# Optimization experiments

Hardware: AMD Instinct MI355X
Metric: run time of the kernel (lower is better)

The kernel has to match this reference:

```python
import jax, jax.numpy as jnp
from jax import lax
import numpy as np

B, T, F = 2048, 1000, 40
H1, H2 = 8, 6


def _p(key, shape, fan):
    # uniform(-1/sqrt(fan), 1/sqrt(fan)) like torch LSTM/Linear init
    bound = 1.0 / np.sqrt(fan)
    return jax.random.uniform(key, shape, jnp.float32, -bound, bound)


def setup_inputs() -> dict:
    key = jax.random.key(0)
    ks = jax.random.split(key, 11)
    return {
        "x": jax.random.normal(ks[0], (B, T, F), jnp.float32),
        "W_ih1": _p(ks[1], (4 * H1, F), H1),
        "W_hh1": _p(ks[2], (4 * H1, H1), H1),
        "b_ih1": _p(ks[3], (4 * H1,), H1),
        "b_hh1": _p(ks[4], (4 * H1,), H1),
        "W_ih2": _p(ks[5], (4 * H2, H1), H2),
        "W_hh2": _p(ks[6], (4 * H2, H2), H2),
        "b_ih2": _p(ks[7], (4 * H2,), H2),
        "b_hh2": _p(ks[8], (4 * H2,), H2),
        "W_fc": _p(ks[9], (1, H2), H2),
        "b_fc": _p(ks[10], (1,), H2),
    }


def lstm_layer(x, W_ih, W_hh, b_ih, b_hh):
    """batch_first unidirectional LSTM; returns all hidden states [B,T,H]."""
    Bb = x.shape[0]
    H = W_hh.shape[1]
    # precompute input-side gate preactivations for all timesteps: [T,B,4H]
    xg = (jnp.einsum('btf,gf->btg', x, W_ih) + b_ih + b_hh).transpose(1, 0, 2)
    W_hh_T = W_hh.T  # [H,4H]

    def step(carry, xg_t):
        h, c = carry
        g = xg_t + h @ W_hh_T  # [B,4H]
        i, f, gcell, o = jnp.split(g, 4, axis=-1)  # torch gate order i,f,g,o
        i = jax.nn.sigmoid(i)
        f = jax.nn.sigmoid(f)
        gcell = jnp.tanh(gcell)
        o = jax.nn.sigmoid(o)
        c = f * c + i * gcell
        h = o * jnp.tanh(c)
        return (h, c), h

    h0 = jnp.zeros((Bb, H), x.dtype)
    c0 = jnp.zeros((Bb, H), x.dtype)
    _, hs = lax.scan(step, (h0, c0), xg)  # hs: [T,B,H]
    return hs.transpose(1, 0, 2)


def reference(x, W_ih1, W_hh1, b_ih1, b_hh1, W_ih2, W_hh2, b_ih2, b_hh2, W_fc, b_fc):
    out = lstm_layer(x, W_ih1, W_hh1, b_ih1, b_hh1)
    out = jnp.tanh(out)
    out = lstm_layer(out, W_ih2, W_hh2, b_ih2, b_hh2)
    out = jnp.tanh(out)
    last = out[:, -1, :]  # [B,H2]
    logits = last @ W_fc.T + b_fc  # [B,1]
    return jax.nn.sigmoid(logits)
```

## Files before the change

kernel.cpp:

```cpp
#include <hip/hip_runtime.h>


constexpr int Bn = 2048, Tn = 1000, Fn = 40;
constexpr int H1n = 8, H2n = 6;
constexpr int TT  = 20;
constexpr int NTt = Tn / TT;
constexpr int BW  = 8;

__device__ __forceinline__ float frcp(float x) { return __builtin_amdgcn_rcpf(x); }
__device__ __forceinline__ float fsig(float x) { return frcp(1.0f + __expf(-x)); }
__device__ __forceinline__ float ftanh(float x) {
    return fmaf(2.0f, frcp(1.0f + __expf(-2.0f * x)), -1.0f);
}

template <int K>
__device__ __forceinline__ float bswz(float v) {
    return __int_as_float(__builtin_amdgcn_ds_swizzle(__float_as_int(v), (K << 5) | 0x18));
}

__global__ __launch_bounds__(256, 1) void lstm_upl(
    const float* __restrict__ x,
    const float* __restrict__ W_ih1, const float* __restrict__ W_hh1,
    const float* __restrict__ b_ih1, const float* __restrict__ b_hh1,
    const float* __restrict__ W_ih2, const float* __restrict__ W_hh2,
    const float* __restrict__ b_ih2, const float* __restrict__ b_hh2,
    const float* __restrict__ W_fc,  const float* __restrict__ b_fc,
    float* __restrict__ out)
{
    __shared__ float s_x [2][BW][TT][Fn];
    __shared__ float s_xg[2][TT][BW][32];

    const int lane  = threadIdx.x & 63;
    const int wslot = __builtin_amdgcn_readfirstlane((int)(threadIdx.x >> 6));
    const int b0    = blockIdx.x * BW;


    if (wslot == 0) {
        const int q  = lane >> 3;
        const int j  = lane & 7;
        const int j2 = (j < H2n) ? j : (H2n - 1);

        float wi1[H1n], wf1[H1n], wg1[H1n], wo1[H1n];
#pragma unroll
        for (int k = 0; k < H1n; ++k) {
            wi1[k] = W_hh1[(     j) * H1n + k];
            wf1[k] = W_hh1[( 8 + j) * H1n + k];
            wg1[k] = W_hh1[(16 + j) * H1n + k];
            wo1[k] = W_hh1[(24 + j) * H1n + k];
        }
        float wi2[H1n], wf2[H1n], wg2[H1n], wo2[H1n];
#pragma unroll
        for (int k = 0; k < H1n; ++k) {
            wi2[k] = W_ih2[(     j2) * H1n + k];
            wf2[k] = W_ih2[( 6 + j2) * H1n + k];
            wg2[k] = W_ih2[(12 + j2) * H1n + k];
            wo2[k] = W_ih2[(18 + j2) * H1n + k];
        }
        float vi2[H2n], vf2[H2n], vg2[H2n], vo2[H2n];
#pragma unroll
        for (int k = 0; k < H2n; ++k) {
            vi2[k] = W_hh2[(     j2) * H2n + k];
            vf2[k] = W_hh2[( 6 + j2) * H2n + k];
            vg2[k] = W_hh2[(12 + j2) * H2n + k];
            vo2[k] = W_hh2[(18 + j2) * H2n + k];
        }
        const float bi2c = b_ih2[     j2] + b_hh2[     j2];
        const float bf2c = b_ih2[ 6 + j2] + b_hh2[ 6 + j2];
        const float bg2c = b_ih2[12 + j2] + b_hh2[12 + j2];
        const float bo2c = b_ih2[18 + j2] + b_hh2[18 + j2];

        float wfc[H2n];
#pragma unroll
        for (int k = 0; k < H2n; ++k) wfc[k] = W_fc[k];
        const float bfc = b_fc[0];

        float c1 = 0.f, c2 = 0.f;
        float h1s[H1n], th1s[H1n], h2s[H2n];
#pragma unroll
        for (int k = 0; k < H1n; ++k) { h1s[k] = 0.f; th1s[k] = 0.f; }
#pragma unroll
        for (int k = 0; k < H2n; ++k) h2s[k] = 0.f;

        const int myoff = q * 32 + j * 4;

        for (int p = 0; p <= NTt + 1; ++p) {
            if (p >= 2) {
                const float* xgt = &s_xg[(p - 2) & 1][0][0][0];
                float4 xg4 = *(const float4*)(xgt + myoff);
                for (int i = 0; i < TT; ++i) {
                    const int in = (i + 1 < TT) ? (i + 1) : i;
                    const float4 xgn = *(const float4*)(xgt + in * (BW * 32) + myoff);

                    float ai0 = xg4.x, ai1 = 0.f, af0 = xg4.y, af1 = 0.f;
                    float ag0 = xg4.z, ag1 = 0.f, ao0 = xg4.w, ao1 = 0.f;
#pragma unroll
                    for (int k = 0; k < H1n; k += 2) {
                        ai0 = fmaf(h1s[k], wi1[k], ai0); ai1 = fmaf(h1s[k+1], wi1[k+1], ai1);
                        af0 = fmaf(h1s[k], wf1[k], af0); af1 = fmaf(h1s[k+1], wf1[k+1], af1);
                        ag0 = fmaf(h1s[k], wg1[k], ag0); ag1 = fmaf(h1s[k+1], wg1[k+1], ag1);
                        ao0 = fmaf(h1s[k], wo1[k], ao0); ao1 = fmaf(h1s[k+1], wo1[k+1], ao1);
                    }
                    const float iv = fsig (ai0 + ai1);
                    const float fv = fsig (af0 + af1);
                    const float gv = ftanh(ag0 + ag1);
                    const float ov = fsig (ao0 + ao1);
                    c1 = fmaf(fv, c1, iv * gv);
                    const float h1v  = ov * ftanh(c1);
                    const float th1v = ftanh(h1v);

                    h1s[0] = bswz<0>(h1v); h1s[1] = bswz<1>(h1v);
                    h1s[2] = bswz<2>(h1v); h1s[3] = bswz<3>(h1v);
                    h1s[4] = bswz<4>(h1v); h1s[5] = bswz<5>(h1v);
                    h1s[6] = bswz<6>(h1v); h1s[7] = bswz<7>(h1v);
                    th1s[0] = bswz<0>(th1v); th1s[1] = bswz<1>(th1v);
                    th1s[2] = bswz<2>(th1v); th1s[3] = bswz<3>(th1v);
                    th1s[4] = bswz<4>(th1v); th1s[5] = bswz<5>(th1v);
                    th1s[6] = bswz<6>(th1v); th1s[7] = bswz<7>(th1v);

                    float bi0 = bi2c, bi1 = 0.f, bf0 = bf2c, bf1 = 0.f;
                    float bg0 = bg2c, bg1 = 0.f, bo0 = bo2c, bo1 = 0.f;
#pragma unroll
                    for (int k = 0; k < H2n; k += 2) {
                        bi0 = fmaf(h2s[k], vi2[k], bi0); bi1 = fmaf(h2s[k+1], vi2[k+1], bi1);
                        bf0 = fmaf(h2s[k], vf2[k], bf0); bf1 = fmaf(h2s[k+1], vf2[k+1], bf1);
                        bg0 = fmaf(h2s[k], vg2[k], bg0); bg1 = fmaf(h2s[k+1], vg2[k+1], bg1);
                        bo0 = fmaf(h2s[k], vo2[k], bo0); bo1 = fmaf(h2s[k+1], vo2[k+1], bo1);
                    }
#pragma unroll
                    for (int k = 0; k < H1n; k += 2) {
                        bi0 = fmaf(th1s[k], wi2[k], bi0); bi1 = fmaf(th1s[k+1], wi2[k+1], bi1);
                        bf0 = fmaf(th1s[k], wf2[k], bf0); bf1 = fmaf(th1s[k+1], wf2[k+1], bf1);
                        bg0 = fmaf(th1s[k], wg2[k], bg0); bg1 = fmaf(th1s[k+1], wg2[k+1], bg1);
                        bo0 = fmaf(th1s[k], wo2[k], bo0); bo1 = fmaf(th1s[k+1], wo2[k+1], bo1);
                    }
                    const float i2v = fsig (bi0 + bi1);
                    const float f2v = fsig (bf0 + bf1);
                    const float g2v = ftanh(bg0 + bg1);
                    const float o2v = fsig (bo0 + bo1);
                    c2 = fmaf(f2v, c2, i2v * g2v);
                    const float h2v = o2v * ftanh(c2);

                    h2s[0] = bswz<0>(h2v); h2s[1] = bswz<1>(h2v);
                    h2s[2] = bswz<2>(h2v); h2s[3] = bswz<3>(h2v);
                    h2s[4] = bswz<4>(h2v); h2s[5] = bswz<5>(h2v);

                    xg4 = xgn;
                }
            }
            __syncthreads();
        }

        if (j == 0) {
            float a = bfc;
#pragma unroll
            for (int k = 0; k < H2n; ++k) a = fmaf(ftanh(h2s[k]), wfc[k], a);
            out[b0 + q] = fsig(a);
        }
    } else {
        const int wp = wslot - 1;
        const int g  = lane & 31;
        const int qh = (lane >> 5) * 4;
        const int jj = g & 7, ss = g >> 3;

        float wih1[Fn];
#pragma unroll
        for (int k = 0; k < Fn; ++k) wih1[k] = W_ih1[g * Fn + k];
        const float bias1 = b_ih1[g] + b_hh1[g];

        const char* xcb = (const char*)x;

        for (int p = 0; p <= NTt + 1; ++p) {
            if (p < NTt) {
                float4 vv[9];
#pragma unroll
                for (int ci = 0; ci < 9; ++ci) {
                    const int c = wp + ci * 3;
                    if (c < 25) {
                        const int o   = c * 1024 + lane * 16;
                        const int qq  = o / 3200;
                        const int rem = o - qq * 3200;
                        vv[ci] = *(const float4*)(xcb
                                   + (size_t)(b0 + qq) * (Tn * Fn * 4)
                                   + (size_t)p * (TT * Fn * 4) + rem);
                    }
                }
                char* ld = (char*)&s_x[p & 1][0][0][0];
#pragma unroll
                for (int ci = 0; ci < 9; ++ci) {
                    const int c = wp + ci * 3;
                    if (c < 25)
                        *(float4*)(ld + c * 1024 + lane * 16) = vv[ci];
                }
            }

            if (p >= 1 && p <= NTt) {
                const float* sx = &s_x [(p - 1) & 1][0][0][0];
                float*       so = &s_xg[(p - 1) & 1][0][0][0];
                for (int r = wp; r < TT; r += 3) {
#pragma unroll
                    for (int qq = 0; qq < 4; ++qq) {
                        const int q = qh + qq;
                        const float* xr = sx + (q * TT + r) * Fn;
                        float a0 = bias1, a1 = 0.f, a2 = 0.f, a3 = 0.f;
#pragma unroll
                        for (int k = 0; k < Fn; k += 4) {
                            const float4 cv = *(const float4*)&xr[k];
                            a0 = fmaf(cv.x, wih1[k],     a0);
                            a1 = fmaf(cv.y, wih1[k + 1], a1);
                            a2 = fmaf(cv.z, wih1[k + 2], a2);
                            a3 = fmaf(cv.w, wih1[k + 3], a3);
                        }
                        so[(r * BW + q) * 32 + jj * 4 + ss] = (a0 + a1) + (a2 + a3);
                    }
                }
            }
            __syncthreads();
        }
    }
}

extern "C" void kernel_launch(void* const* d_in, const int* in_sizes, int n_in,
                              void* d_out, int out_size, void* d_ws, size_t ws_size,
                              hipStream_t stream) {
    (void)in_sizes; (void)n_in; (void)out_size; (void)d_ws; (void)ws_size;
    const float* x     = (const float*)d_in[0];
    const float* W_ih1 = (const float*)d_in[1];
    const float* W_hh1 = (const float*)d_in[2];
    const float* b_ih1 = (const float*)d_in[3];
    const float* b_hh1 = (const float*)d_in[4];
    const float* W_ih2 = (const float*)d_in[5];
    const float* W_hh2 = (const float*)d_in[6];
    const float* b_ih2 = (const float*)d_in[7];
    const float* b_hh2 = (const float*)d_in[8];
    const float* W_fc  = (const float*)d_in[9];
    const float* b_fc  = (const float*)d_in[10];
    float* out = (float*)d_out;

    lstm_upl<<<dim3(Bn / BW), dim3(256), 0, stream>>>(x, W_ih1, W_hh1, b_ih1, b_hh1,
                                                      W_ih2, W_hh2, b_ih2, b_hh2,
                                                      W_fc, b_fc, out);
}
```

Measured before the change: 794.2 us.

## Pad x tile rows, compute four gates per lane, overlap x loads with GEMV

```diff
diff --git a/kernel.cpp b/kernel.cpp
--- a/kernel.cpp
+++ b/kernel.cpp
@@ -6,6 +6,11 @@
 constexpr int TT  = 20;
 constexpr int NTt = Tn / TT;
 constexpr int BW  = 8;
+
+constexpr int SROWF  = TT * Fn + 4;
+constexpr int SXF    = BW * SROWF;
+constexpr int SXB    = SXF * 4;
+constexpr int NCHUNK = (SXB + 1023) / 1024;
 
 __device__ __forceinline__ float frcp(float x) { return __builtin_amdgcn_rcpf(x); }
 __device__ __forceinline__ float fsig(float x) { return frcp(1.0f + __expf(-x)); }
@@ -27,8 +32,8 @@
     const float* __restrict__ W_fc,  const float* __restrict__ b_fc,
     float* __restrict__ out)
 {
-    __shared__ float s_x [2][BW][TT][Fn];
-    __shared__ float s_xg[2][TT][BW][32];
+    __shared__ float s_x [2][SXF];
+    __shared__ float s_xg[2][TT * BW * 32];
 
     const int lane  = threadIdx.x & 63;
     const int wslot = __builtin_amdgcn_readfirstlane((int)(threadIdx.x >> 6));
@@ -85,7 +90,7 @@
 
         for (int p = 0; p <= NTt + 1; ++p) {
             if (p >= 2) {
-                const float* xgt = &s_xg[(p - 2) & 1][0][0][0];
+                const float* xgt = &s_xg[(p - 2) & 1][0];
                 float4 xg4 = *(const float4*)(xgt + myoff);
                 for (int i = 0; i < TT; ++i) {
                     const int in = (i + 1 < TT) ? (i + 1) : i;
@@ -158,59 +163,82 @@
         }
     } else {
         const int wp = wslot - 1;
-        const int g  = lane & 31;
-        const int qh = (lane >> 5) * 4;
-        const int jj = g & 7, ss = g >> 3;
-
-        float wih1[Fn];
-#pragma unroll
-        for (int k = 0; k < Fn; ++k) wih1[k] = W_ih1[g * Fn + k];
-        const float bias1 = b_ih1[g] + b_hh1[g];
+        const int q  = lane >> 3;
+        const int j  = lane & 7;
+
+        float wI[Fn], wF[Fn], wG[Fn], wO[Fn];
+#pragma unroll
+        for (int k = 0; k < Fn; ++k) {
+            wI[k] = W_ih1[(     j) * Fn + k];
+            wF[k] = W_ih1[( 8 + j) * Fn + k];
+            wG[k] = W_ih1[(16 + j) * Fn + k];
+            wO[k] = W_ih1[(24 + j) * Fn + k];
+        }
+        const float bI = b_ih1[     j] + b_hh1[     j];
+        const float bF = b_ih1[ 8 + j] + b_hh1[ 8 + j];
+        const float bG = b_ih1[16 + j] + b_hh1[16 + j];
+        const float bO = b_ih1[24 + j] + b_hh1[24 + j];
 
         const char* xcb = (const char*)x;
 
         for (int p = 0; p <= NTt + 1; ++p) {
+            float4 vv[9];
             if (p < NTt) {
-                float4 vv[9];
 #pragma unroll
                 for (int ci = 0; ci < 9; ++ci) {
                     const int c = wp + ci * 3;
-                    if (c < 25) {
-                        const int o   = c * 1024 + lane * 16;
-                        const int qq  = o / 3200;
-                        const int rem = o - qq * 3200;
-                        vv[ci] = *(const float4*)(xcb
-                                   + (size_t)(b0 + qq) * (Tn * Fn * 4)
-                                   + (size_t)p * (TT * Fn * 4) + rem);
-                    }
-                }
-                char* ld = (char*)&s_x[p & 1][0][0][0];
+                    if (c < NCHUNK) {
+                        const int o = c * 1024 + lane * 16;
+                        if (o < SXB) {
+                            const int qq  = o / (SROWF * 4);
+                            int       rem = o - qq * (SROWF * 4);
+                            if (rem > TT * Fn * 4 - 16) rem = TT * Fn * 4 - 16;
+                            vv[ci] = *(const float4*)(xcb
+                                       + (size_t)(b0 + qq) * (Tn * Fn * 4)
+                                       + (size_t)p * (TT * Fn * 4) + rem);
+                        }
+                    }
+                }
+            }
+
+            if (p >= 1 && p <= NTt) {
+                const float* xq = &s_x[(p - 1) & 1][0] + q * SROWF;
+                float*       so = &s_xg[(p - 1) & 1][0];
+                for (int r = wp; r < TT; r += 3) {
+                    const float* xr = xq + r * Fn;
+                    float i0 = bI, i1 = 0.f, i2 = 0.f, i3 = 0.f;
+                    float f0 = bF, f1 = 0.f, f2 = 0.f, f3 = 0.f;
+                    float g0 = bG, g1 = 0.f, g2 = 0.f, g3 = 0.f;
+                    float o0 = bO, o1 = 0.f, o2 = 0.f, o3 = 0.f;
+#pragma unroll
+                    for (int k = 0; k < Fn; k += 4) {
+                        const float4 cv = *(const float4*)&xr[k];
+                        i0 = fmaf(cv.x, wI[k],     i0); i1 = fmaf(cv.y, wI[k + 1], i1);
+                        i2 = fmaf(cv.z, wI[k + 2], i2); i3 = fmaf(cv.w, wI[k + 3], i3);
+                        f0 = fmaf(cv.x, wF[k],     f0); f1 = fmaf(cv.y, wF[k + 1], f1);
+                        f2 = fmaf(cv.z, wF[k + 2], f2); f3 = fmaf(cv.w, wF[k + 3], f3);
+                        g0 = fmaf(cv.x, wG[k],     g0); g1 = fmaf(cv.y, wG[k + 1], g1);
+                        g2 = fmaf(cv.z, wG[k + 2], g2); g3 = fmaf(cv.w, wG[k + 3], g3);
+                        o0 = fmaf(cv.x, wO[k],     o0); o1 = fmaf(cv.y, wO[k + 1], o1);
+                        o2 = fmaf(cv.z, wO[k + 2], o2); o3 = fmaf(cv.w, wO[k + 3], o3);
+                    }
+                    float4 r4;
+                    r4.x = (i0 + i1) + (i2 + i3);
+                    r4.y = (f0 + f1) + (f2 + f3);
+                    r4.z = (g0 + g1) + (g2 + g3);
+                    r4.w = (o0 + o1) + (o2 + o3);
+                    *(float4*)&so[(r * BW + q) * 32 + j * 4] = r4;
+                }
+            }
+
+            if (p < NTt) {
+                char* ld = (char*)&s_x[p & 1][0];
 #pragma unroll
                 for (int ci = 0; ci < 9; ++ci) {
                     const int c = wp + ci * 3;
-                    if (c < 25)
-                        *(float4*)(ld + c * 1024 + lane * 16) = vv[ci];
-                }
-            }
-
-            if (p >= 1 && p <= NTt) {
-                const float* sx = &s_x [(p - 1) & 1][0][0][0];
-                float*       so = &s_xg[(p - 1) & 1][0][0][0];
-                for (int r = wp; r < TT; r += 3) {
-#pragma unroll
-                    for (int qq = 0; qq < 4; ++qq) {
-                        const int q = qh + qq;
-                        const float* xr = sx + (q * TT + r) * Fn;
-                        float a0 = bias1, a1 = 0.f, a2 = 0.f, a3 = 0.f;
-#pragma unroll
-                        for (int k = 0; k < Fn; k += 4) {
-                            const float4 cv = *(const float4*)&xr[k];
-                            a0 = fmaf(cv.x, wih1[k],     a0);
-                            a1 = fmaf(cv.y, wih1[k + 1], a1);
-                            a2 = fmaf(cv.z, wih1[k + 2], a2);
-                            a3 = fmaf(cv.w, wih1[k + 3], a3);
-                        }
-                        so[(r * BW + q) * 32 + jj * 4 + ss] = (a0 + a1) + (a2 + a3);
+                    if (c < NCHUNK) {
+                        const int o = c * 1024 + lane * 16;
+                        if (o < SXB) *(float4*)(ld + o) = vv[ci];
                     }
                 }
             }
```

Result: faster. 727.9 us (-8.3%).
